# Kernel optimization log

Measured on AMD Instinct MI355X. Metric: run time of the kernel, lower is better.

The kernel has to match this reference:

```python
import jax, jax.numpy as jnp
import numpy as np

B, LAT, FCON, NCOND = 1024, 64, 256, 1
HID, E, GATE_H = 512, 8, 64
FREC, NFUT = 256, 2
IN_SZ = LAT + FCON * NCOND          # 320
INTER = LAT + HID                   # 576
OUT_SZ = NFUT * FREC                # 512


def setup_inputs() -> dict:
    key = jax.random.key(0)
    ks = jax.random.split(key, 16)

    def kaiming(k, shape):
        # kaiming_uniform over fan_in = shape[-2] (matches torch init on [E, in, out])
        fan_in = shape[-2]
        bound = np.sqrt(6.0 / fan_in)
        return jax.random.uniform(k, shape, jnp.float32, -bound, bound)

    def lin(kw, kb, din, dout):
        bound = 1.0 / np.sqrt(din)
        w = jax.random.uniform(kw, (din, dout), jnp.float32, -bound, bound)
        b = jax.random.uniform(kb, (dout,), jnp.float32, -bound, bound)
        return w, b

    gw1, gb1 = lin(ks[0], ks[1], IN_SZ, GATE_H)
    gw2, gb2 = lin(ks[2], ks[3], GATE_H, GATE_H)
    gw3, gb3 = lin(ks[4], ks[5], GATE_H, E)

    return {
        "z": jax.random.normal(ks[6], (B, LAT), jnp.float32),
        "c": jax.random.normal(ks[7], (B, FCON * NCOND), jnp.float32),
        "w0": kaiming(ks[8], (E, IN_SZ, HID)),
        "b0": jnp.full((E, HID), 0.01, jnp.float32),
        "w1": kaiming(ks[9], (E, INTER, HID)),
        "b1": jnp.full((E, HID), 0.01, jnp.float32),
        "w2": kaiming(ks[10], (E, INTER, OUT_SZ)),
        "b2": jnp.full((E, OUT_SZ), 0.01, jnp.float32),
        "gw1": gw1, "gb1": gb1,
        "gw2": gw2, "gb2": gb2,
        "gw3": gw3, "gb3": gb3,
    }


def _moe_layer(coeff, z, layer_out, w, b, act):
    # math identical to: mixed_w = coeff @ flat(w); baddbmm(mixed_b, inp, mixed_w)
    # expressed as a fused contraction (no [B, in, out] materialization)
    inp = jnp.concatenate((z, layer_out), axis=1)          # [B, in]
    out = jnp.einsum('bi,eio,be->bo', inp, w, coeff)       # [B, out]
    out = out + coeff @ b                                  # mixed bias
    return act(out) if act is not None else out


def reference(z, c, w0, b0, w1, b1, w2, b2, gw1, gb1, gw2, gb2, gw3, gb3):
    x = jnp.concatenate((z, c), axis=1)                    # [B, IN_SZ]
    h = jax.nn.elu(x @ gw1 + gb1)
    h = jax.nn.elu(h @ gw2 + gb2)
    coeff = jax.nn.softmax(h @ gw3 + gb3, axis=1)          # [B, E]

    out = _moe_layer(coeff, z, c, w0, b0, jax.nn.elu)      # [B, HID]
    out = _moe_layer(coeff, z, out, w1, b1, jax.nn.elu)    # [B, HID]
    out = _moe_layer(coeff, z, out, w2, b2, None)          # [B, OUT_SZ]
    return out
```

## Files before the change

### kernel.cpp

```cpp
#include <hip/hip_runtime.h>
#include <hip/hip_bf16.h>
#include <stdint.h>
#include <math.h>

#define B_    1024
#define LAT   64
#define FCON  256
#define IN_SZ 320
#define HID   512
#define E_    8
#define GH    64
#define INTER 576
#define OUT_SZ 512
#define NTOT  4096
#define KI0   10
#define KI12  18

typedef __attribute__((ext_vector_type(8))) __bf16 bf16x8;
typedef __attribute__((ext_vector_type(4))) float  f32x4;

__device__ __forceinline__ float elu_f(float x) { return x > 0.f ? x : expf(x) - 1.f; }
__device__ __forceinline__ __bf16 to_bf16(float f) {
    __hip_bfloat16 h = __float2bfloat16(f);
    return *reinterpret_cast<__bf16*>(&h);
}

__device__ __forceinline__ void async_ld16(const void* g, void* l) {
    __builtin_amdgcn_global_load_lds(
        (const __attribute__((address_space(1))) unsigned int*)g,
        (__attribute__((address_space(3))) unsigned int*)l,
        16, 0, 0);
}


#define PREP_GATE 64
#define PREP_ZC   (PREP_GATE + 160)
#define PREP_W0   (PREP_ZC + 8 * KI0 * 2)
#define PREP_W1   (PREP_W0 + 8 * KI12 * 2)
#define PREP_W2   (PREP_W1 + 8 * KI12 * 2)
#define PREP_ALL  PREP_W2

#define WPAD 261
#define SMEM_F (32 * WPAD)

__device__ __forceinline__ void do_zcpack(
    int bx, const float* __restrict__ z, const float* __restrict__ c,
    bf16x8* __restrict__ Ap0, bf16x8* __restrict__ Ap1, bf16x8* __restrict__ Ap2)
{
    const int wid  = bx * 4 + (threadIdx.x >> 6);
    const int lane = threadIdx.x & 63, q = lane >> 4, r = lane & 15;
    bf16x8 v;
    if (wid < 128) {
        const int mi = wid >> 1, ki = wid & 1;
        const float* src = z + (size_t)(mi * 16 + r) * LAT + ki * 32 + q * 8;
        const f32x4 lo = *(const f32x4*)src, hi = *(const f32x4*)(src + 4);
#pragma unroll
        for (int j = 0; j < 4; j++) { v[j] = to_bf16(lo[j]); v[j + 4] = to_bf16(hi[j]); }
        Ap0[((size_t)mi * KI0  + ki) * 64 + lane] = v;
        Ap1[((size_t)mi * KI12 + ki) * 64 + lane] = v;
        Ap2[((size_t)mi * KI12 + ki) * 64 + lane] = v;
    } else {
        const int cid = wid - 128;
        const int mi = cid >> 3, ki = 2 + (cid & 7);
        const float* src = c + (size_t)(mi * 16 + r) * FCON + (ki - 2) * 32 + q * 8;
        const f32x4 lo = *(const f32x4*)src, hi = *(const f32x4*)(src + 4);
#pragma unroll
        for (int j = 0; j < 4; j++) { v[j] = to_bf16(lo[j]); v[j + 4] = to_bf16(hi[j]); }
        Ap0[((size_t)mi * KI0 + ki) * 64 + lane] = v;
    }
}

__device__ __forceinline__ void do_wpack2(
    int f, const float* __restrict__ w, bf16x8* __restrict__ Wp, int KI,
    float* __restrict__ lds)
{
    const int e = f / (2 * KI), rem = f % (2 * KI);
    const int ki = rem >> 1, ot2 = rem & 1;
    const int K = KI * 32;
    const float* base = w + ((size_t)e * K + ki * 32) * 512 + ot2 * 256;

#pragma unroll
    for (int p = 0; p < 8; ++p) {
        const int idx = p * 256 + threadIdx.x;
        const int kl = idx >> 6, c4 = idx & 63;
        const f32x4 v = *(const f32x4*)(base + (size_t)kl * 512 + c4 * 4);
        float* d = lds + kl * WPAD + c4 * 4;
        d[0] = v[0]; d[1] = v[1]; d[2] = v[2]; d[3] = v[3];
    }
    __syncthreads();

    const int wv = threadIdx.x >> 6, lane = threadIdx.x & 63;
    const int q = lane >> 4, r = lane & 15;
#pragma unroll
    for (int ff = 0; ff < 4; ++ff) {
        const int fo = wv * 4 + ff;
        const int ol = fo * 16 + r;
        bf16x8 v;
#pragma unroll
        for (int j = 0; j < 8; ++j) v[j] = to_bf16(lds[(q * 8 + j) * WPAD + ol]);
        const int ni = e * 32 + ot2 * 16 + fo;
        Wp[((size_t)ni * KI + ki) * 64 + lane] = v;
    }
}

__device__ __forceinline__ void do_gate(
    int bx, const float* __restrict__ z, const float* __restrict__ c,
    const float* __restrict__ gw1, const float* __restrict__ gb1,
    const float* __restrict__ gw2, const float* __restrict__ gb2,
    const float* __restrict__ gw3, const float* __restrict__ gb3,
    float* __restrict__ coeff, float* __restrict__ smem)
{
    float* xs = smem;
    float* h  = smem + 16 * 320;
    const int r0 = bx * 16;
    const int wave = threadIdx.x >> 6, lane = threadIdx.x & 63;

#pragma unroll
    for (int p = 0; p < 5; ++p) {
        const int idx = p * 256 + threadIdx.x;
        const int row = idx / 80, c4 = idx % 80;
        const float* src = (c4 < 16)
            ? (z + (size_t)(r0 + row) * LAT  + c4 * 4)
            : (c + (size_t)(r0 + row) * FCON + (c4 - 16) * 4);
        *(f32x4*)(xs + row * 320 + c4 * 4) = *(const f32x4*)src;
    }
    __syncthreads();

    float a0, a1, a2, a3;
    {
        const float b = gb1[lane];
        a0 = b; a1 = b; a2 = b; a3 = b;
        const float* x0 = xs + (wave * 4 + 0) * 320;
        const float* x1 = xs + (wave * 4 + 1) * 320;
        const float* x2 = xs + (wave * 4 + 2) * 320;
        const float* x3 = xs + (wave * 4 + 3) * 320;
#pragma unroll 8
        for (int i = 0; i < IN_SZ; ++i) {
            const float wv = gw1[i * GH + lane];
            a0 = fmaf(x0[i], wv, a0);
            a1 = fmaf(x1[i], wv, a1);
            a2 = fmaf(x2[i], wv, a2);
            a3 = fmaf(x3[i], wv, a3);
        }
        h[(wave * 4 + 0) * GH + lane] = elu_f(a0);
        h[(wave * 4 + 1) * GH + lane] = elu_f(a1);
        h[(wave * 4 + 2) * GH + lane] = elu_f(a2);
        h[(wave * 4 + 3) * GH + lane] = elu_f(a3);
    }
    {
        const float b = gb2[lane];
        a0 = b; a1 = b; a2 = b; a3 = b;
        const float* h0 = h + (wave * 4 + 0) * GH;
        const float* h1 = h + (wave * 4 + 1) * GH;
        const float* h2 = h + (wave * 4 + 2) * GH;
        const float* h3 = h + (wave * 4 + 3) * GH;
#pragma unroll 8
        for (int i = 0; i < GH; ++i) {
            const float wv = gw2[i * GH + lane];
            a0 = fmaf(h0[i], wv, a0);
            a1 = fmaf(h1[i], wv, a1);
            a2 = fmaf(h2[i], wv, a2);
            a3 = fmaf(h3[i], wv, a3);
        }
        h[(wave * 4 + 0) * GH + lane] = elu_f(a0);
        h[(wave * 4 + 1) * GH + lane] = elu_f(a1);
        h[(wave * 4 + 2) * GH + lane] = elu_f(a2);
        h[(wave * 4 + 3) * GH + lane] = elu_f(a3);
    }
    if (lane < 32) {
        const int rloc = lane >> 3, e = lane & 7;
        const float* hr = h + (wave * 4 + rloc) * GH;
        float lg = gb3[e];
#pragma unroll 8
        for (int i = 0; i < GH; ++i) lg = fmaf(hr[i], gw3[i * E_ + e], lg);
        float mx = lg;
        mx = fmaxf(mx, __shfl_xor(mx, 1, 8));
        mx = fmaxf(mx, __shfl_xor(mx, 2, 8));
        mx = fmaxf(mx, __shfl_xor(mx, 4, 8));
        const float ex = expf(lg - mx);
        float sm = ex;
        sm += __shfl_xor(sm, 1, 8);
        sm += __shfl_xor(sm, 2, 8);
        sm += __shfl_xor(sm, 4, 8);
        coeff[(size_t)(r0 + wave * 4 + rloc) * E_ + e] = ex / sm;
    }
}

__global__ __launch_bounds__(256) void prep_kernel(
    const float* __restrict__ z, const float* __restrict__ c,
    const float* __restrict__ w0, const float* __restrict__ w1,
    const float* __restrict__ w2,
    const float* __restrict__ gw1, const float* __restrict__ gb1,
    const float* __restrict__ gw2, const float* __restrict__ gb2,
    const float* __restrict__ gw3, const float* __restrict__ gb3,
    bf16x8* __restrict__ Ap0, bf16x8* __restrict__ Ap1, bf16x8* __restrict__ Ap2,
    bf16x8* __restrict__ Wp0, bf16x8* __restrict__ Wp1, bf16x8* __restrict__ Wp2,
    float* __restrict__ coeff)
{
    __shared__ float smem[SMEM_F];
    const int bx = blockIdx.x;
    if (bx < PREP_GATE) {
        do_gate(bx, z, c, gw1, gb1, gw2, gb2, gw3, gb3, coeff, smem);
    } else if (bx < PREP_ZC) {
        do_zcpack(bx - PREP_GATE, z, c, Ap0, Ap1, Ap2);
    } else if (bx < PREP_W0) {
        do_wpack2(bx - PREP_ZC, w0, Wp0, KI0, smem);
    } else if (bx < PREP_W1) {
        do_wpack2(bx - PREP_W0, w1, Wp1, KI12, smem);
    } else {
        do_wpack2(bx - PREP_W1, w2, Wp2, KI12, smem);
    }
}

template<int KI, int FINAL>
__global__ __launch_bounds__(256) void layer_kernel(
    const bf16x8* __restrict__ Ap, const bf16x8* __restrict__ Wp,
    const float* __restrict__ coeff, const float* __restrict__ bias,
    __bf16* __restrict__ ApN, float* __restrict__ fout)
{
    constexpr int NS = KI / 2;
    __shared__ bf16x8 bs[2][2][E_][64];
    const int lane = threadIdx.x & 63, w = threadIdx.x >> 6;
    const int q = lane >> 4, r = lane & 15;
    const int o0 = blockIdx.x * 16;
    const int nt = blockIdx.x;
    const int mi = blockIdx.y * 4 + w;

    const bf16x8* aB = Ap + (size_t)mi * KI * 64 + lane;
    const int e0 = w * 2;

    f32x4 acc[E_];
#pragma unroll
    for (int e = 0; e < E_; e++) acc[e] = (f32x4){0.f, 0.f, 0.f, 0.f};

#define STAGE(s_, buf_)                                                        \
    {                                                                          \
        _Pragma("unroll")                                                      \
        for (int kk = 0; kk < 2; ++kk) {                                       \
            _Pragma("unroll")                                                  \
            for (int t = 0; t < 2; ++t) {                                      \
                const int e = e0 + t;                                          \
                const bf16x8* g = Wp +                                         \
                    ((size_t)e * 32 * KI + (size_t)nt * KI + ((s_) * 2 + kk)) * 64 + lane; \
                async_ld16((const void*)g, (void*)&bs[buf_][kk][e][0]);        \
            }                                                                  \
        }                                                                      \
    }

    STAGE(0, 0);
    bf16x8 af0 = aB[0], af1 = aB[64];

    int cur = 0;
#pragma unroll
    for (int s = 0; s < NS; ++s) {
        bf16x8 afn0 = af0, afn1 = af1;
        if (s + 1 < NS) {
            STAGE(s + 1, cur ^ 1);
            afn0 = aB[(size_t)(s * 2 + 2) * 64];
            afn1 = aB[(size_t)(s * 2 + 3) * 64];
            asm volatile("s_waitcnt vmcnt(6)" ::: "memory");
        } else {
            asm volatile("s_waitcnt vmcnt(0)" ::: "memory");
        }
        __builtin_amdgcn_s_barrier();
        __builtin_amdgcn_sched_barrier(0);

#pragma unroll
        for (int kk = 0; kk < 2; ++kk) {
            const bf16x8 af = kk ? af1 : af0;
            bf16x8 bfr[E_];
#pragma unroll
            for (int e = 0; e < E_; e++) bfr[e] = bs[cur][kk][e][lane];
#pragma unroll
            for (int e = 0; e < E_; e++)
                acc[e] = __builtin_amdgcn_mfma_f32_16x16x32_bf16(af, bfr[e], acc[e], 0, 0, 0);
        }

        __builtin_amdgcn_sched_barrier(0);
        __builtin_amdgcn_s_barrier();
        af0 = afn0; af1 = afn1; cur ^= 1;
    }
#undef STAGE

    float be[E_];
#pragma unroll
    for (int e = 0; e < E_; e++) be[e] = bias[(size_t)e * 512 + o0 + r];

#pragma unroll
    for (int v = 0; v < 4; v++) {
        const int row = mi * 16 + q * 4 + v;
        const float* cr = coeff + (size_t)row * E_;
        const f32x4 clo = *(const f32x4*)cr, chi = *(const f32x4*)(cr + 4);
        float sv = 0.f;
#pragma unroll
        for (int e = 0; e < 4; e++) sv += clo[e] * (acc[e][v] + be[e]);
#pragma unroll
        for (int e = 0; e < 4; e++) sv += chi[e] * (acc[4 + e][v] + be[4 + e]);
        if (FINAL) {
            fout[(size_t)row * OUT_SZ + o0 + r] = sv;
        } else {
            const float hh = elu_f(sv);
            const int k  = LAT + o0 + r;
            const int ki2 = k >> 5, kq2 = (k & 31) >> 3, jb2 = k & 7;
            ApN[(((size_t)mi * KI12 + ki2) * 64 + kq2 * 16 + (q * 4 + v)) * 8 + jb2] =
                to_bf16(hh);
        }
    }
}

static inline size_t align256(size_t x) { return (x + 255) & ~(size_t)255; }

extern "C" void kernel_launch(void* const* d_in, const int* in_sizes, int n_in,
                              void* d_out, int out_size, void* d_ws, size_t ws_size,
                              hipStream_t stream)
{
    const float* z   = (const float*)d_in[0];
    const float* c   = (const float*)d_in[1];
    const float* w0  = (const float*)d_in[2];
    const float* b0  = (const float*)d_in[3];
    const float* w1  = (const float*)d_in[4];
    const float* b1  = (const float*)d_in[5];
    const float* w2  = (const float*)d_in[6];
    const float* b2  = (const float*)d_in[7];
    const float* gw1 = (const float*)d_in[8];
    const float* gb1 = (const float*)d_in[9];
    const float* gw2 = (const float*)d_in[10];
    const float* gb2 = (const float*)d_in[11];
    const float* gw3 = (const float*)d_in[12];
    const float* gb3 = (const float*)d_in[13];
    float* out = (float*)d_out;

    uint8_t* p = (uint8_t*)d_ws;
    bf16x8* Wp0 = (bf16x8*)p; p += align256((size_t)NTOT * IN_SZ * 2);
    bf16x8* Wp1 = (bf16x8*)p; p += align256((size_t)NTOT * INTER * 2);
    bf16x8* Wp2 = (bf16x8*)p; p += align256((size_t)NTOT * INTER * 2);
    bf16x8* Ap0 = (bf16x8*)p; p += align256((size_t)B_ * IN_SZ * 2);
    bf16x8* Ap1 = (bf16x8*)p; p += align256((size_t)B_ * INTER * 2);
    bf16x8* Ap2 = (bf16x8*)p; p += align256((size_t)B_ * INTER * 2);
    float* coeff = (float*)p; p += align256((size_t)B_ * E_ * 4);

    prep_kernel<<<PREP_ALL, 256, 0, stream>>>(
        z, c, w0, w1, w2, gw1, gb1, gw2, gb2, gw3, gb3,
        Ap0, Ap1, Ap2, Wp0, Wp1, Wp2, coeff);

    layer_kernel<KI0, 0><<<dim3(32, 16), 256, 0, stream>>>(
        Ap0, Wp0, coeff, b0, (__bf16*)Ap1, nullptr);
    layer_kernel<KI12, 0><<<dim3(32, 16), 256, 0, stream>>>(
        Ap1, Wp1, coeff, b1, (__bf16*)Ap2, nullptr);
    layer_kernel<KI12, 1><<<dim3(32, 16), 256, 0, stream>>>(
        Ap2, Wp2, coeff, b2, nullptr, out);
}
```

Baseline: 136.4 us.

## Switch layer GEMMs to 32x32x16 MFMA with per-wave expert split and LDS reduction

Repacks activations and weights into 32-row/32-column fragments with 16-wide K steps so each layer can use the 32x32x16 bf16 MFMA. Each wave now owns two experts over a 32x32 output tile and covers the full M tile, instead of each wave owning its own 16-row slice across all eight experts. The per-wave partial mixes are reduced across waves through a new LDS buffer. The aim is fewer MFMA issues and fewer LDS reads of B fragments per output, at the cost of an extra LDS reduction, a barrier, and a changed grid shape.

```diff
diff --git a/kernel.cpp b/kernel.cpp
--- a/kernel.cpp
+++ b/kernel.cpp
@@ -15,9 +15,13 @@
 #define NTOT  4096
 #define KI0   10
 #define KI12  18
-
-typedef __attribute__((ext_vector_type(8))) __bf16 bf16x8;
-typedef __attribute__((ext_vector_type(4))) float  f32x4;
+#define KF0   20
+#define KF12  36
+
+typedef __attribute__((ext_vector_type(8)))  __bf16 bf16x8;
+typedef __attribute__((ext_vector_type(4)))  float  f32x4;
+typedef __attribute__((ext_vector_type(2)))  float  f32x2;
+typedef __attribute__((ext_vector_type(16))) float  f32x16;
 
 __device__ __forceinline__ float elu_f(float x) { return x > 0.f ? x : expf(x) - 1.f; }
 __device__ __forceinline__ __bf16 to_bf16(float f) {
@@ -48,35 +52,39 @@
     bf16x8* __restrict__ Ap0, bf16x8* __restrict__ Ap1, bf16x8* __restrict__ Ap2)
 {
     const int wid  = bx * 4 + (threadIdx.x >> 6);
-    const int lane = threadIdx.x & 63, q = lane >> 4, r = lane & 15;
+    const int lane = threadIdx.x & 63;
+    const int rloc = lane & 31, kq = lane >> 5;
     bf16x8 v;
     if (wid < 128) {
-        const int mi = wid >> 1, ki = wid & 1;
-        const float* src = z + (size_t)(mi * 16 + r) * LAT + ki * 32 + q * 8;
+        const int mi = wid >> 2, kf = wid & 3;
+        const int row = mi * 32 + rloc;
+        const float* src = z + (size_t)row * LAT + kf * 16 + kq * 8;
         const f32x4 lo = *(const f32x4*)src, hi = *(const f32x4*)(src + 4);
 #pragma unroll
         for (int j = 0; j < 4; j++) { v[j] = to_bf16(lo[j]); v[j + 4] = to_bf16(hi[j]); }
-        Ap0[((size_t)mi * KI0  + ki) * 64 + lane] = v;
-        Ap1[((size_t)mi * KI12 + ki) * 64 + lane] = v;
-        Ap2[((size_t)mi * KI12 + ki) * 64 + lane] = v;
+        Ap0[((size_t)mi * KF0  + kf) * 64 + lane] = v;
+        Ap1[((size_t)mi * KF12 + kf) * 64 + lane] = v;
+        Ap2[((size_t)mi * KF12 + kf) * 64 + lane] = v;
     } else {
         const int cid = wid - 128;
-        const int mi = cid >> 3, ki = 2 + (cid & 7);
-        const float* src = c + (size_t)(mi * 16 + r) * FCON + (ki - 2) * 32 + q * 8;
+        const int mi = cid >> 4, kf4 = cid & 15;
+        const int row = mi * 32 + rloc;
+        const float* src = c + (size_t)row * FCON + kf4 * 16 + kq * 8;
         const f32x4 lo = *(const f32x4*)src, hi = *(const f32x4*)(src + 4);
 #pragma unroll
         for (int j = 0; j < 4; j++) { v[j] = to_bf16(lo[j]); v[j + 4] = to_bf16(hi[j]); }
-        Ap0[((size_t)mi * KI0 + ki) * 64 + lane] = v;
+        Ap0[((size_t)mi * KF0 + 4 + kf4) * 64 + lane] = v;
     }
 }
 
 __device__ __forceinline__ void do_wpack2(
-    int f, const float* __restrict__ w, bf16x8* __restrict__ Wp, int KI,
+    int f, const float* __restrict__ w, bf16x8* __restrict__ Wp,
+    int KI32, int KF,
     float* __restrict__ lds)
 {
-    const int e = f / (2 * KI), rem = f % (2 * KI);
+    const int e = f / (2 * KI32), rem = f % (2 * KI32);
     const int ki = rem >> 1, ot2 = rem & 1;
-    const int K = KI * 32;
+    const int K = KI32 * 32;
     const float* base = w + ((size_t)e * K + ki * 32) * 512 + ot2 * 256;
 
 #pragma unroll
@@ -90,16 +98,17 @@
     __syncthreads();
 
     const int wv = threadIdx.x >> 6, lane = threadIdx.x & 63;
-    const int q = lane >> 4, r = lane & 15;
+    const int cloc = lane & 31, kq = lane >> 5;
 #pragma unroll
     for (int ff = 0; ff < 4; ++ff) {
-        const int fo = wv * 4 + ff;
-        const int ol = fo * 16 + r;
+        const int fi = wv * 4 + ff;
+        const int kfl = fi >> 3, ot_loc = fi & 7;
         bf16x8 v;
 #pragma unroll
-        for (int j = 0; j < 8; ++j) v[j] = to_bf16(lds[(q * 8 + j) * WPAD + ol]);
-        const int ni = e * 32 + ot2 * 16 + fo;
-        Wp[((size_t)ni * KI + ki) * 64 + lane] = v;
+        for (int j = 0; j < 8; ++j)
+            v[j] = to_bf16(lds[(kfl * 16 + kq * 8 + j) * WPAD + ot_loc * 32 + cloc]);
+        const int ni = e * 16 + ot2 * 8 + ot_loc;
+        Wp[((size_t)ni * KF + ki * 2 + kfl) * 64 + lane] = v;
     }
 }
 
@@ -197,52 +206,52 @@
     bf16x8* __restrict__ Wp0, bf16x8* __restrict__ Wp1, bf16x8* __restrict__ Wp2,
     float* __restrict__ coeff)
 {
-    __shared__ float smem[SMEM_F];
+    __shared__ __align__(16) float smem[SMEM_F];
     const int bx = blockIdx.x;
     if (bx < PREP_GATE) {
         do_gate(bx, z, c, gw1, gb1, gw2, gb2, gw3, gb3, coeff, smem);
     } else if (bx < PREP_ZC) {
         do_zcpack(bx - PREP_GATE, z, c, Ap0, Ap1, Ap2);
     } else if (bx < PREP_W0) {
-        do_wpack2(bx - PREP_ZC, w0, Wp0, KI0, smem);
+        do_wpack2(bx - PREP_ZC, w0, Wp0, KI0, KF0, smem);
     } else if (bx < PREP_W1) {
-        do_wpack2(bx - PREP_W0, w1, Wp1, KI12, smem);
+        do_wpack2(bx - PREP_W0, w1, Wp1, KI12, KF12, smem);
     } else {
-        do_wpack2(bx - PREP_W1, w2, Wp2, KI12, smem);
-    }
-}
-
-template<int KI, int FINAL>
+        do_wpack2(bx - PREP_W1, w2, Wp2, KI12, KF12, smem);
+    }
+}
+
+template<int KF, int FINAL>
 __global__ __launch_bounds__(256) void layer_kernel(
     const bf16x8* __restrict__ Ap, const bf16x8* __restrict__ Wp,
     const float* __restrict__ coeff, const float* __restrict__ bias,
     __bf16* __restrict__ ApN, float* __restrict__ fout)
 {
-    constexpr int NS = KI / 2;
+    constexpr int NS = KF / 2;
     __shared__ bf16x8 bs[2][2][E_][64];
+    __shared__ float  red[4][16][64];
     const int lane = threadIdx.x & 63, w = threadIdx.x >> 6;
-    const int q = lane >> 4, r = lane & 15;
-    const int o0 = blockIdx.x * 16;
+    const int cloc = lane & 31;
     const int nt = blockIdx.x;
-    const int mi = blockIdx.y * 4 + w;
-
-    const bf16x8* aB = Ap + (size_t)mi * KI * 64 + lane;
+    const int o0 = nt * 32;
+    const int mi = blockIdx.y;
+    const int m0 = mi * 32;
     const int e0 = w * 2;
 
-    f32x4 acc[E_];
-#pragma unroll
-    for (int e = 0; e < E_; e++) acc[e] = (f32x4){0.f, 0.f, 0.f, 0.f};
+    const bf16x8* aB = Ap + (size_t)mi * KF * 64 + lane;
+
+    f32x16 acc0 = {}, acc1 = {};
 
 #define STAGE(s_, buf_)                                                        \
     {                                                                          \
         _Pragma("unroll")                                                      \
-        for (int kk = 0; kk < 2; ++kk) {                                       \
+        for (int kfl = 0; kfl < 2; ++kfl) {                                    \
             _Pragma("unroll")                                                  \
             for (int t = 0; t < 2; ++t) {                                      \
                 const int e = e0 + t;                                          \
                 const bf16x8* g = Wp +                                         \
-                    ((size_t)e * 32 * KI + (size_t)nt * KI + ((s_) * 2 + kk)) * 64 + lane; \
-                async_ld16((const void*)g, (void*)&bs[buf_][kk][e][0]);        \
+                    ((size_t)(e * 16 + nt) * KF + ((s_) * 2 + kfl)) * 64 + lane; \
+                async_ld16((const void*)g, (void*)&bs[buf_][kfl][e][0]);       \
             }                                                                  \
         }                                                                      \
     }
@@ -265,16 +274,12 @@
         __builtin_amdgcn_s_barrier();
         __builtin_amdgcn_sched_barrier(0);
 
-#pragma unroll
-        for (int kk = 0; kk < 2; ++kk) {
-            const bf16x8 af = kk ? af1 : af0;
-            bf16x8 bfr[E_];
-#pragma unroll
-            for (int e = 0; e < E_; e++) bfr[e] = bs[cur][kk][e][lane];
-#pragma unroll
-            for (int e = 0; e < E_; e++)
-                acc[e] = __builtin_amdgcn_mfma_f32_16x16x32_bf16(af, bfr[e], acc[e], 0, 0, 0);
-        }
+        const bf16x8 b00 = bs[cur][0][e0][lane],     b01 = bs[cur][0][e0 + 1][lane];
+        const bf16x8 b10 = bs[cur][1][e0][lane],     b11 = bs[cur][1][e0 + 1][lane];
+        acc0 = __builtin_amdgcn_mfma_f32_32x32x16_bf16(af0, b00, acc0, 0, 0, 0);
+        acc1 = __builtin_amdgcn_mfma_f32_32x32x16_bf16(af0, b01, acc1, 0, 0, 0);
+        acc0 = __builtin_amdgcn_mfma_f32_32x32x16_bf16(af1, b10, acc0, 0, 0, 0);
+        acc1 = __builtin_amdgcn_mfma_f32_32x32x16_bf16(af1, b11, acc1, 0, 0, 0);
 
         __builtin_amdgcn_sched_barrier(0);
         __builtin_amdgcn_s_barrier();
@@ -282,28 +287,33 @@
     }
 #undef STAGE
 
-    float be[E_];
-#pragma unroll
-    for (int e = 0; e < E_; e++) be[e] = bias[(size_t)e * 512 + o0 + r];
-
-#pragma unroll
-    for (int v = 0; v < 4; v++) {
-        const int row = mi * 16 + q * 4 + v;
-        const float* cr = coeff + (size_t)row * E_;
-        const f32x4 clo = *(const f32x4*)cr, chi = *(const f32x4*)(cr + 4);
-        float sv = 0.f;
-#pragma unroll
-        for (int e = 0; e < 4; e++) sv += clo[e] * (acc[e][v] + be[e]);
-#pragma unroll
-        for (int e = 0; e < 4; e++) sv += chi[e] * (acc[4 + e][v] + be[4 + e]);
+    const float be0 = bias[(size_t)e0 * 512 + o0 + cloc];
+    const float be1 = bias[(size_t)(e0 + 1) * 512 + o0 + cloc];
+
+    const int rbase = m0 + 4 * (lane >> 5);
+#pragma unroll
+    for (int reg = 0; reg < 16; ++reg) {
+        const int row = rbase + (reg & 3) + 8 * (reg >> 2);
+        const f32x2 cv = *(const f32x2*)(coeff + (size_t)row * E_ + e0);
+        red[w][reg][lane] = cv[0] * (acc0[reg] + be0) + cv[1] * (acc1[reg] + be1);
+    }
+    __syncthreads();
+
+#pragma unroll
+    for (int rr = 0; rr < 4; ++rr) {
+        const int reg = w * 4 + rr;
+        const int row = rbase + (reg & 3) + 8 * (reg >> 2);
+        const float sv = red[0][reg][lane] + red[1][reg][lane]
+                       + red[2][reg][lane] + red[3][reg][lane];
+        const int col = o0 + cloc;
         if (FINAL) {
-            fout[(size_t)row * OUT_SZ + o0 + r] = sv;
+            fout[(size_t)row * OUT_SZ + col] = sv;
         } else {
             const float hh = elu_f(sv);
-            const int k  = LAT + o0 + r;
-            const int ki2 = k >> 5, kq2 = (k & 31) >> 3, jb2 = k & 7;
-            ApN[(((size_t)mi * KI12 + ki2) * 64 + kq2 * 16 + (q * 4 + v)) * 8 + jb2] =
-                to_bf16(hh);
+            const int k = LAT + col;
+            const int kf2 = k >> 4, j2 = k & 15;
+            ApN[(((size_t)mi * KF12 + kf2) * 64 + (row - m0) + 32 * (j2 >> 3)) * 8
+                + (j2 & 7)] = to_bf16(hh);
         }
     }
 }
@@ -343,10 +353,10 @@
         z, c, w0, w1, w2, gw1, gb1, gw2, gb2, gw3, gb3,
         Ap0, Ap1, Ap2, Wp0, Wp1, Wp2, coeff);
 
-    layer_kernel<KI0, 0><<<dim3(32, 16), 256, 0, stream>>>(
+    layer_kernel<KF0, 0><<<dim3(16, 32), 256, 0, stream>>>(
         Ap0, Wp0, coeff, b0, (__bf16*)Ap1, nullptr);
-    layer_kernel<KI12, 0><<<dim3(32, 16), 256, 0, stream>>>(
+    layer_kernel<KF12, 0><<<dim3(16, 32), 256, 0, stream>>>(
         Ap1, Wp1, coeff, b1, (__bf16*)Ap2, nullptr);
-    layer_kernel<KI12, 1><<<dim3(32, 16), 256, 0, stream>>>(
+    layer_kernel<KF12, 1><<<dim3(16, 32), 256, 0, stream>>>(
         Ap2, Wp2, coeff, b2, nullptr, out);
 }
```

Result: slower. 144.4 us (+5.9%).
